# Optimization experiments

Measured on AMD Instinct MI355X. Metric: run time of the kernel, lower is better.

Reference implementation:

```python
import jax, jax.numpy as jnp
import numpy as np

N_NODES = 50000
N_EDGES = 400000
IN_DIM, HID_DIM, OUT_DIM = 512, 512, 128


def sage_conv(x, src, dst, W_l, b_l, W_r, n_nodes):
    # PyG SAGEConv (mean aggr): out = lin_l(mean_{j in N(i)} x_j) + lin_r(x_i)
    msgs = x[src]                                             # [E, d_in]
    agg = jax.ops.segment_sum(msgs, dst, num_segments=n_nodes)
    deg = jax.ops.segment_sum(jnp.ones((src.shape[0],), x.dtype), dst,
                              num_segments=n_nodes)
    mean = agg / jnp.maximum(deg, 1.0)[:, None]
    return mean @ W_l + b_l + x @ W_r


def setup_inputs() -> dict:
    key = jax.random.key(0)
    ks = jax.random.split(key, 9)
    x = jax.random.normal(ks[0], (N_NODES, IN_DIM), dtype=jnp.float32)
    edge_index = jax.random.randint(ks[1], (2, N_EDGES), 0, N_NODES, dtype=jnp.int32)

    def glorot(k, d_in, d_out):
        s = (6.0 / (d_in + d_out)) ** 0.5
        return jax.random.uniform(k, (d_in, d_out), jnp.float32, -s, s)

    return {
        "x": x,
        "edge_index": edge_index,
        "W1_l": glorot(ks[2], IN_DIM, HID_DIM),
        "b1": jnp.zeros((HID_DIM,), jnp.float32),
        "W1_r": glorot(ks[3], IN_DIM, HID_DIM),
        "W2_l": glorot(ks[4], HID_DIM, HID_DIM),
        "b2": jnp.zeros((HID_DIM,), jnp.float32),
        "W2_r": glorot(ks[5], HID_DIM, HID_DIM),
        "W3_l": glorot(ks[6], HID_DIM, OUT_DIM),
        "b3": jnp.zeros((OUT_DIM,), jnp.float32),
        "W3_r": glorot(ks[7], HID_DIM, OUT_DIM),
    }


def reference(x, edge_index, W1_l, b1, W1_r, W2_l, b2, W2_r, W3_l, b3, W3_r):
    src, dst = edge_index[0], edge_index[1]
    n = x.shape[0]
    h = sage_conv(x, src, dst, W1_l, b1, W1_r, n)
    h = jax.nn.relu(h)  # dropout is identity in eval mode
    h = sage_conv(h, src, dst, W2_l, b2, W2_r, n)
    h = jax.nn.relu(h)
    h = sage_conv(h, src, dst, W3_l, b3, W3_r, n)
    return jax.nn.log_softmax(h, axis=-1)
```

## Files before the change

### kernel.cpp

```cpp
#include <hip/hip_runtime.h>
#include <hip/hip_bf16.h>


#define N_NODES 50000
#define N_EDGES 400000

typedef unsigned short u16;
typedef unsigned int u32;
typedef __attribute__((ext_vector_type(8))) short short8;
typedef __attribute__((ext_vector_type(4))) float floatx4;

#define ASYNC16(g, l)                                                      \
    __builtin_amdgcn_global_load_lds(                                      \
        (const __attribute__((address_space(1))) void*)(g),                \
        (__attribute__((address_space(3))) void*)(l), 16, 0, 0)

__device__ __forceinline__ u16 f32_to_bf16(float f) {
    u32 u = __float_as_uint(f);
    u32 r = 0x7FFFu + ((u >> 16) & 1u);
    return (u16)((u + r) >> 16);
}
__device__ __forceinline__ float bf16_to_f32(u32 lo16) {
    return __uint_as_float(lo16 << 16);
}

__global__ __launch_bounds__(256) void zero4_kernel(float4* __restrict__ p, int n4) {
    int i = blockIdx.x * 256 + threadIdx.x;
    if (i < n4) p[i] = make_float4(0.f, 0.f, 0.f, 0.f);
}

__global__ __launch_bounds__(256) void hist_kernel(const int* __restrict__ dst,
                                                   int* __restrict__ deg, int E) {
    int e = blockIdx.x * 256 + threadIdx.x;
    if (e < E) atomicAdd(&deg[dst[e]], 1);
}

__global__ __launch_bounds__(256) void scan_reduce(const int* __restrict__ v,
                                                   int* __restrict__ bsums, int n) {
    __shared__ int sh[256];
    int i = blockIdx.x * 256 + threadIdx.x;
    sh[threadIdx.x] = (i < n) ? v[i] : 0;
    __syncthreads();
    for (int off = 128; off > 0; off >>= 1) {
        if (threadIdx.x < off) sh[threadIdx.x] += sh[threadIdx.x + off];
        __syncthreads();
    }
    if (threadIdx.x == 0) bsums[blockIdx.x] = sh[0];
}

__global__ __launch_bounds__(256) void scan_sums(int* __restrict__ bsums, int nb) {
    __shared__ int sh[256];
    int t = threadIdx.x;
    int val = (t < nb) ? bsums[t] : 0;
    sh[t] = val;
    __syncthreads();
    for (int off = 1; off < 256; off <<= 1) {
        int v = (t >= off) ? sh[t - off] : 0;
        __syncthreads();
        sh[t] += v;
        __syncthreads();
    }
    if (t < nb) bsums[t] = sh[t] - val;
}

__global__ __launch_bounds__(256) void scan_final(int* __restrict__ v,
                                                  const int* __restrict__ bsums, int n) {
    __shared__ int sh[256];
    int t = threadIdx.x;
    int i = blockIdx.x * 256 + t;
    int val = (i < n) ? v[i] : 0;
    sh[t] = val;
    __syncthreads();
    for (int off = 1; off < 256; off <<= 1) {
        int x = (t >= off) ? sh[t - off] : 0;
        __syncthreads();
        sh[t] += x;
        __syncthreads();
    }
    int excl = sh[t] - val + bsums[blockIdx.x];
    if (i < n) v[i] = excl;
    if (i == n - 1) v[n] = excl + val;
}

__global__ __launch_bounds__(256) void fill_kernel(const int* __restrict__ src,
                                                   const int* __restrict__ dst,
                                                   const int* __restrict__ row_start,
                                                   int* __restrict__ cursor,
                                                   int* __restrict__ csr_src, int E) {
    int e = blockIdx.x * 256 + threadIdx.x;
    if (e < E) {
        int d = dst[e];
        int pos = row_start[d] + atomicAdd(&cursor[d], 1);
        csr_src[pos] = src[e];
    }
}

__global__ __launch_bounds__(256) void convert_bf16(const float* __restrict__ in,
                                                    u16* __restrict__ out, int n8) {
    int i = blockIdx.x * 256 + threadIdx.x;
    if (i >= n8) return;
    const float4* p = (const float4*)in + (size_t)i * 2;
    float4 v0 = p[0], v1 = p[1];
    uint4 o;
    o.x = (u32)f32_to_bf16(v0.x) | ((u32)f32_to_bf16(v0.y) << 16);
    o.y = (u32)f32_to_bf16(v0.z) | ((u32)f32_to_bf16(v0.w) << 16);
    o.z = (u32)f32_to_bf16(v1.x) | ((u32)f32_to_bf16(v1.y) << 16);
    o.w = (u32)f32_to_bf16(v1.z) | ((u32)f32_to_bf16(v1.w) << 16);
    ((uint4*)out)[i] = o;
}

__global__ __launch_bounds__(256) void transpose_w(const float* __restrict__ W,
                                                   u16* __restrict__ WT,
                                                   int K, int N) {
    __shared__ float t[32][33];
    int n0 = blockIdx.x * 32, k0 = blockIdx.y * 32;
    int c = threadIdx.x & 31, r0 = threadIdx.x >> 5;
    for (int r = r0; r < 32; r += 8)
        t[r][c] = W[(size_t)(k0 + r) * N + n0 + c];
    __syncthreads();
    for (int r = r0; r < 32; r += 8)
        WT[(size_t)(n0 + r) * K + k0 + c] = f32_to_bf16(t[c][r]);
}

__global__ __launch_bounds__(256) void gemm_bf16(
    const u16* __restrict__ A, const u16* __restrict__ BT,
    u16* __restrict__ Cl, u16* __restrict__ Cr,
    int M, int split, int nStrips, int nCols) {
    __shared__ u16 As[2][4096];
    __shared__ u16 Bs[2][4096];

    const int grp = 8 * nCols;
    int b = blockIdx.x;
    int strip = (b / grp) * 8 + (b & 7);
    int colt = (b % grp) >> 3;
    if (strip >= nStrips) return;
    const int row0 = strip * 128, col0 = colt * 128;

    const int t = threadIdx.x;
    const int w = t >> 6, lane = t & 63;
    const int wm = (w >> 1) * 64, wn = (w & 1) * 64;
    const int l15 = lane & 15, kq = lane >> 4;
    const int swz = (l15 >> 1) & 3;

    floatx4 acc[4][4];
#pragma unroll
    for (int i = 0; i < 4; ++i)
#pragma unroll
        for (int j = 0; j < 4; ++j) acc[i][j] = floatx4{0.f, 0.f, 0.f, 0.f};

    const int sr = t >> 2;
    const int sc = t & 3;
    const int swzS = (sr >> 1) & 3;
    const size_t aA0 = (size_t)min(row0 + sr, M - 1) * 512 + (sc ^ swzS) * 8;
    const size_t aA1 = (size_t)min(row0 + 64 + sr, M - 1) * 512 + (sc ^ swzS) * 8;
    const size_t aB0 = (size_t)(col0 + sr) * 512 + (sc ^ swzS) * 8;
    const size_t aB1 = (size_t)(col0 + 64 + sr) * 512 + (sc ^ swzS) * 8;
    const int d0 = w * 512;
    const int d1 = 2048 + w * 512;

    auto stage = [&](int it, int buf) {
        const int eff = it * 32;
        ASYNC16(A + aA0 + eff, &As[buf][d0]);
        ASYNC16(A + aA1 + eff, &As[buf][d1]);
        ASYNC16(BT + aB0 + eff, &Bs[buf][d0]);
        ASYNC16(BT + aB1 + eff, &Bs[buf][d1]);
    };

    stage(0, 0);
    __syncthreads();
    for (int it = 0; it < 16; ++it) {
        const int buf = it & 1;
        if (it + 1 < 16) stage(it + 1, buf ^ 1);

        const int kc = (kq ^ swz) * 8;
        short8 a[4], bfr[4];
#pragma unroll
        for (int mt = 0; mt < 4; ++mt)
            a[mt] = *(const short8*)&As[buf][(wm + mt * 16 + l15) * 32 + kc];
#pragma unroll
        for (int nt = 0; nt < 4; ++nt)
            bfr[nt] = *(const short8*)&Bs[buf][(wn + nt * 16 + l15) * 32 + kc];
#pragma unroll
        for (int mt = 0; mt < 4; ++mt)
#pragma unroll
            for (int nt = 0; nt < 4; ++nt)
                acc[mt][nt] = __builtin_amdgcn_mfma_f32_16x16x32_bf16(
                    bfr[nt], a[mt], acc[mt][nt], 0, 0, 0);
        __syncthreads();
    }

    u16* __restrict__ Cbase = (col0 < split) ? Cl : Cr;
    const int cadj = (col0 < split) ? col0 : (col0 - split);
#pragma unroll
    for (int mt = 0; mt < 4; ++mt) {
        int row = row0 + wm + mt * 16 + l15;
        if (row >= M) continue;
#pragma unroll
        for (int nt = 0; nt < 4; ++nt) {
            int c0 = cadj + wn + nt * 16 + kq * 4;
            uint2 o;
            o.x = (u32)f32_to_bf16(acc[mt][nt][0]) |
                  ((u32)f32_to_bf16(acc[mt][nt][1]) << 16);
            o.y = (u32)f32_to_bf16(acc[mt][nt][2]) |
                  ((u32)f32_to_bf16(acc[mt][nt][3]) << 16);
            *(uint2*)(Cbase + (size_t)row * split + c0) = o;
        }
    }
}

__device__ __forceinline__ void acc8(float* a, uint4 v) {
    a[0] += bf16_to_f32(v.x & 0xffffu); a[1] += bf16_to_f32(v.x >> 16);
    a[2] += bf16_to_f32(v.y & 0xffffu); a[3] += bf16_to_f32(v.y >> 16);
    a[4] += bf16_to_f32(v.z & 0xffffu); a[5] += bf16_to_f32(v.z >> 16);
    a[6] += bf16_to_f32(v.w & 0xffffu); a[7] += bf16_to_f32(v.w >> 16);
}

__global__ __launch_bounds__(256) void gather_add_relu512(
    const u16* __restrict__ Yl, const u16* __restrict__ Yr,
    const float* __restrict__ bias,
    const int* __restrict__ row_start, const int* __restrict__ csr_src,
    u16* __restrict__ h, int M) {
    int node = (blockIdx.x * 256 + threadIdx.x) >> 6;
    int lane = threadIdx.x & 63;
    if (node >= M) return;
    int beg = row_start[node], end = row_start[node + 1];
    float a[8] = {0.f, 0.f, 0.f, 0.f, 0.f, 0.f, 0.f, 0.f};
    for (int c = beg; c < end; c += 64) {
        int nb = min(64, end - c);
        int eid = (lane < nb) ? csr_src[c + lane] : 0;
        int i = 0;
        for (; i + 4 <= nb; i += 4) {
            int s0 = __shfl(eid, i);
            int s1 = __shfl(eid, i + 1);
            int s2 = __shfl(eid, i + 2);
            int s3 = __shfl(eid, i + 3);
            uint4 v0 = ((const uint4*)(Yl + (size_t)s0 * 512))[lane];
            uint4 v1 = ((const uint4*)(Yl + (size_t)s1 * 512))[lane];
            uint4 v2 = ((const uint4*)(Yl + (size_t)s2 * 512))[lane];
            uint4 v3 = ((const uint4*)(Yl + (size_t)s3 * 512))[lane];
            acc8(a, v0); acc8(a, v1); acc8(a, v2); acc8(a, v3);
        }
        for (; i < nb; ++i) {
            int s = __shfl(eid, i);
            uint4 v = ((const uint4*)(Yl + (size_t)s * 512))[lane];
            acc8(a, v);
        }
    }
    float inv = 1.0f / fmaxf((float)(end - beg), 1.0f);
    uint4 yr = ((const uint4*)(Yr + (size_t)node * 512))[lane];
    float4 b0 = ((const float4*)bias)[lane * 2];
    float4 b1 = ((const float4*)bias)[lane * 2 + 1];
    float v0 = fmaxf(a[0] * inv + bf16_to_f32(yr.x & 0xffffu) + b0.x, 0.f);
    float v1 = fmaxf(a[1] * inv + bf16_to_f32(yr.x >> 16)     + b0.y, 0.f);
    float v2 = fmaxf(a[2] * inv + bf16_to_f32(yr.y & 0xffffu) + b0.z, 0.f);
    float v3 = fmaxf(a[3] * inv + bf16_to_f32(yr.y >> 16)     + b0.w, 0.f);
    float v4 = fmaxf(a[4] * inv + bf16_to_f32(yr.z & 0xffffu) + b1.x, 0.f);
    float v5 = fmaxf(a[5] * inv + bf16_to_f32(yr.z >> 16)     + b1.y, 0.f);
    float v6 = fmaxf(a[6] * inv + bf16_to_f32(yr.w & 0xffffu) + b1.z, 0.f);
    float v7 = fmaxf(a[7] * inv + bf16_to_f32(yr.w >> 16)     + b1.w, 0.f);
    uint4 o;
    o.x = (u32)f32_to_bf16(v0) | ((u32)f32_to_bf16(v1) << 16);
    o.y = (u32)f32_to_bf16(v2) | ((u32)f32_to_bf16(v3) << 16);
    o.z = (u32)f32_to_bf16(v4) | ((u32)f32_to_bf16(v5) << 16);
    o.w = (u32)f32_to_bf16(v6) | ((u32)f32_to_bf16(v7) << 16);
    ((uint4*)(h + (size_t)node * 512))[lane] = o;
}

__global__ __launch_bounds__(256) void gather_add_lsm128(
    const u16* __restrict__ Yl, const u16* __restrict__ Yr,
    const float* __restrict__ bias,
    const int* __restrict__ row_start, const int* __restrict__ csr_src,
    float* __restrict__ out, int M) {
    int node = blockIdx.x * 16 + (threadIdx.x >> 4);
    int lane = threadIdx.x & 63;
    int li = lane & 15;
    int gbase = lane & 48;
    if (node >= M) return;
    int beg = row_start[node], end = row_start[node + 1];
    float a[8] = {0.f, 0.f, 0.f, 0.f, 0.f, 0.f, 0.f, 0.f};
    for (int c = beg; c < end; c += 16) {
        int nb = min(16, end - c);
        int eid = (li < nb) ? csr_src[c + li] : 0;
        int i = 0;
        for (; i + 4 <= nb; i += 4) {
            int s0 = __shfl(eid, gbase + i);
            int s1 = __shfl(eid, gbase + i + 1);
            int s2 = __shfl(eid, gbase + i + 2);
            int s3 = __shfl(eid, gbase + i + 3);
            uint4 v0 = ((const uint4*)(Yl + (size_t)s0 * 128))[li];
            uint4 v1 = ((const uint4*)(Yl + (size_t)s1 * 128))[li];
            uint4 v2 = ((const uint4*)(Yl + (size_t)s2 * 128))[li];
            uint4 v3 = ((const uint4*)(Yl + (size_t)s3 * 128))[li];
            acc8(a, v0); acc8(a, v1); acc8(a, v2); acc8(a, v3);
        }
        for (; i < nb; ++i) {
            int s = __shfl(eid, gbase + i);
            uint4 v = ((const uint4*)(Yl + (size_t)s * 128))[li];
            acc8(a, v);
        }
    }
    float inv = 1.0f / fmaxf((float)(end - beg), 1.0f);
    uint4 yr = ((const uint4*)(Yr + (size_t)node * 128))[li];
    float4 b0 = ((const float4*)bias)[li * 2];
    float4 b1 = ((const float4*)bias)[li * 2 + 1];
    float v[8];
    v[0] = a[0] * inv + bf16_to_f32(yr.x & 0xffffu) + b0.x;
    v[1] = a[1] * inv + bf16_to_f32(yr.x >> 16)     + b0.y;
    v[2] = a[2] * inv + bf16_to_f32(yr.y & 0xffffu) + b0.z;
    v[3] = a[3] * inv + bf16_to_f32(yr.y >> 16)     + b0.w;
    v[4] = a[4] * inv + bf16_to_f32(yr.z & 0xffffu) + b1.x;
    v[5] = a[5] * inv + bf16_to_f32(yr.z >> 16)     + b1.y;
    v[6] = a[6] * inv + bf16_to_f32(yr.w & 0xffffu) + b1.z;
    v[7] = a[7] * inv + bf16_to_f32(yr.w >> 16)     + b1.w;
    float m = v[0];
#pragma unroll
    for (int j = 1; j < 8; ++j) m = fmaxf(m, v[j]);
#pragma unroll
    for (int off = 1; off < 16; off <<= 1) m = fmaxf(m, __shfl_xor(m, off));
    float s = 0.f;
#pragma unroll
    for (int j = 0; j < 8; ++j) s += expf(v[j] - m);
#pragma unroll
    for (int off = 1; off < 16; off <<= 1) s += __shfl_xor(s, off);
    float ls = m + logf(s);
    float* p = out + (size_t)node * 128 + li * 8;
    *(float4*)p       = make_float4(v[0] - ls, v[1] - ls, v[2] - ls, v[3] - ls);
    *(float4*)(p + 4) = make_float4(v[4] - ls, v[5] - ls, v[6] - ls, v[7] - ls);
}

extern "C" void kernel_launch(void* const* d_in, const int* in_sizes, int n_in,
                              void* d_out, int out_size, void* d_ws, size_t ws_size,
                              hipStream_t stream) {
    const float* x    = (const float*)d_in[0];
    const int*   ei   = (const int*)d_in[1];
    const float* W1_l = (const float*)d_in[2];
    const float* b1   = (const float*)d_in[3];
    const float* W1_r = (const float*)d_in[4];
    const float* W2_l = (const float*)d_in[5];
    const float* b2   = (const float*)d_in[6];
    const float* W2_r = (const float*)d_in[7];
    const float* W3_l = (const float*)d_in[8];
    const float* b3   = (const float*)d_in[9];
    const float* W3_r = (const float*)d_in[10];
    float* out = (float*)d_out;

    const int* src = ei;
    const int* dst = ei + N_EDGES;

    char* base = (char*)d_ws;
    int* row_start = (int*)(base);
    int* cursor    = (int*)(base + 200208);
    int* bsums     = (int*)(base + 400416);
    int* csr_src   = (int*)(base + 402464);
    u16* xb  = (u16*)(base + 2002464);
    u16* h1b = (u16*)(base + 53202464);
    u16* h2b = (u16*)(base + 104402464);
    u16* Yl  = (u16*)(base + 155602464);
    u16* Yr  = (u16*)(base + 206802464);
    u16* w1T = (u16*)(base + 258002464);
    u16* w2T = (u16*)(base + 259051040);
    u16* w3T = (u16*)(base + 260099616);

    const int E = N_EDGES, M = N_NODES;
    const int nblk = (M + 255) / 256;

    zero4_kernel<<<(25154 + 255) / 256, 256, 0, stream>>>((float4*)d_ws, 25154);
    hist_kernel<<<(E + 255) / 256, 256, 0, stream>>>(dst, row_start, E);
    scan_reduce<<<nblk, 256, 0, stream>>>(row_start, bsums, M);
    scan_sums<<<1, 256, 0, stream>>>(bsums, nblk);
    scan_final<<<nblk, 256, 0, stream>>>(row_start, bsums, M);
    fill_kernel<<<(E + 255) / 256, 256, 0, stream>>>(src, dst, row_start, cursor,
                                                     csr_src, E);

    convert_bf16<<<(3200000 + 255) / 256, 256, 0, stream>>>(x, xb, 3200000);
    transpose_w<<<dim3(16, 16), 256, 0, stream>>>(W1_l, w1T, 512, 512);
    transpose_w<<<dim3(16, 16), 256, 0, stream>>>(W1_r, w1T + 512 * 512, 512, 512);
    transpose_w<<<dim3(16, 16), 256, 0, stream>>>(W2_l, w2T, 512, 512);
    transpose_w<<<dim3(16, 16), 256, 0, stream>>>(W2_r, w2T + 512 * 512, 512, 512);
    transpose_w<<<dim3(4, 16), 256, 0, stream>>>(W3_l, w3T, 512, 128);
    transpose_w<<<dim3(4, 16), 256, 0, stream>>>(W3_r, w3T + 128 * 512, 512, 128);

    const int nStrips = (M + 127) / 128;
    const int grid8 = ((nStrips + 7) / 8) * 64;
    const int grid2 = ((nStrips + 7) / 8) * 16;
    const int gblocks = (M * 64 + 255) / 256;
    const int g16blocks = (M + 15) / 16;

    gemm_bf16<<<grid8, 256, 0, stream>>>(xb, w1T, Yl, Yr, M, 512, nStrips, 8);
    gather_add_relu512<<<gblocks, 256, 0, stream>>>(Yl, Yr, b1, row_start,
                                                    csr_src, h1b, M);
    gemm_bf16<<<grid8, 256, 0, stream>>>(h1b, w2T, Yl, Yr, M, 512, nStrips, 8);
    gather_add_relu512<<<gblocks, 256, 0, stream>>>(Yl, Yr, b2, row_start,
                                                    csr_src, h2b, M);
    gemm_bf16<<<grid2, 256, 0, stream>>>(h2b, w3T, Yl, Yr, M, 128, nStrips, 2);
    gather_add_lsm128<<<g16blocks, 256, 0, stream>>>(Yl, Yr, b3, row_start,
                                                     csr_src, out, M);
}
```

Measured before the change: 656.9 us.

## Replace 128x128 GEMM with 256x256 tile, 512-thread, K=64 pipelined kernel

Replaces the 128x128-tile, 256-thread bf16 MFMA GEMM with a 256x256-tile, 512-thread (8 wave) kernel that stages K=64 slices into 128KB of dynamic LDS. Async global-to-LDS loads for the next slices are interleaved across four sub-phases of the MFMA loop with explicit vmcnt waits and barriers, and s_setprio raises priority around the MFMA bursts. The larger tile is meant to raise arithmetic intensity and cut global/LDS traffic per FLOP. In exchange it uses more registers and LDS, which may limit occupancy, and the third layer's 256-column output now has blocks straddling the Yl/Yr split. Tail rows waste more work because of the bigger strips.

```diff
diff --git a/kernel.cpp b/kernel.cpp
--- a/kernel.cpp
+++ b/kernel.cpp
@@ -122,88 +122,121 @@
         WT[(size_t)(n0 + r) * K + k0 + c] = f32_to_bf16(t[c][r]);
 }
 
-__global__ __launch_bounds__(256) void gemm_bf16(
+__global__ __launch_bounds__(512, 2) void gemm256(
     const u16* __restrict__ A, const u16* __restrict__ BT,
     u16* __restrict__ Cl, u16* __restrict__ Cr,
     int M, int split, int nStrips, int nCols) {
-    __shared__ u16 As[2][4096];
-    __shared__ u16 Bs[2][4096];
+    extern __shared__ u16 lds[];
 
     const int grp = 8 * nCols;
     int b = blockIdx.x;
     int strip = (b / grp) * 8 + (b & 7);
     int colt = (b % grp) >> 3;
     if (strip >= nStrips) return;
-    const int row0 = strip * 128, col0 = colt * 128;
+    const int row0 = strip * 256, col0 = colt * 256;
 
     const int t = threadIdx.x;
     const int w = t >> 6, lane = t & 63;
-    const int wm = (w >> 1) * 64, wn = (w & 1) * 64;
+    const int arow = (w >> 2) * 128;
+    const int bcol = (w & 3) * 64;
     const int l15 = lane & 15, kq = lane >> 4;
-    const int swz = (l15 >> 1) & 3;
-
-    floatx4 acc[4][4];
-#pragma unroll
-    for (int i = 0; i < 4; ++i)
+    const int rchunk = (kq ^ ((l15 >> 1) & 3)) * 8;
+
+    floatx4 acc[8][4];
+#pragma unroll
+    for (int i = 0; i < 8; ++i)
 #pragma unroll
         for (int j = 0; j < 4; ++j) acc[i][j] = floatx4{0.f, 0.f, 0.f, 0.f};
 
-    const int sr = t >> 2;
-    const int sc = t & 3;
-    const int swzS = (sr >> 1) & 3;
-    const size_t aA0 = (size_t)min(row0 + sr, M - 1) * 512 + (sc ^ swzS) * 8;
-    const size_t aA1 = (size_t)min(row0 + 64 + sr, M - 1) * 512 + (sc ^ swzS) * 8;
-    const size_t aB0 = (size_t)(col0 + sr) * 512 + (sc ^ swzS) * 8;
-    const size_t aB1 = (size_t)(col0 + 64 + sr) * 512 + (sc ^ swzS) * 8;
-    const int d0 = w * 512;
-    const int d1 = 2048 + w * 512;
-
-    auto stage = [&](int it, int buf) {
-        const int eff = it * 32;
-        ASYNC16(A + aA0 + eff, &As[buf][d0]);
-        ASYNC16(A + aA1 + eff, &As[buf][d1]);
-        ASYNC16(BT + aB0 + eff, &Bs[buf][d0]);
-        ASYNC16(BT + aB1 + eff, &Bs[buf][d1]);
+    auto stA = [&](int kt2, int i) {
+        const int rb = (w & 3) * 16 + (i & 1) * 64 + (w >> 2) * 128;
+        const int plane = i >> 1;
+        const size_t src = (size_t)min(row0 + rb + (lane >> 2), M - 1) * 512
+                         + kt2 * 64 + plane * 32
+                         + (((lane & 3) ^ ((lane >> 3) & 3)) * 8);
+        const int dst = (kt2 & 1) * 32768 + plane * 8192 + rb * 32;
+        ASYNC16(A + src, &lds[dst]);
     };
-
-    stage(0, 0);
-    __syncthreads();
-    for (int it = 0; it < 16; ++it) {
-        const int buf = it & 1;
-        if (it + 1 < 16) stage(it + 1, buf ^ 1);
-
-        const int kc = (kq ^ swz) * 8;
-        short8 a[4], bfr[4];
-#pragma unroll
-        for (int mt = 0; mt < 4; ++mt)
-            a[mt] = *(const short8*)&As[buf][(wm + mt * 16 + l15) * 32 + kc];
+    auto stB = [&](int kt2, int i) {
+        const int rb = (w & 3) * 16 + (i & 1) * 64 + (w >> 2) * 128;
+        const int plane = i >> 1;
+        const size_t src = (size_t)(col0 + rb + (lane >> 2)) * 512
+                         + kt2 * 64 + plane * 32
+                         + (((lane & 3) ^ ((lane >> 3) & 3)) * 8);
+        const int dst = (kt2 & 1) * 32768 + 16384 + plane * 8192 + rb * 32;
+        ASYNC16(BT + src, &lds[dst]);
+    };
+
+    stA(0, 0); stA(0, 1); stA(0, 2); stA(0, 3);
+    stB(0, 0); stB(0, 1); stB(0, 2); stB(0, 3);
+    stA(1, 0); stA(1, 2);
+    asm volatile("s_waitcnt vmcnt(2)" ::: "memory");
+    __builtin_amdgcn_s_barrier();
+
+    for (int kt = 0; kt < 8; ++kt) {
+        const int sA = (kt & 1) * 32768;
+        const int sB = sA + 16384;
+
+        short8 bfr[4][2];
 #pragma unroll
         for (int nt = 0; nt < 4; ++nt)
-            bfr[nt] = *(const short8*)&Bs[buf][(wn + nt * 16 + l15) * 32 + kc];
-#pragma unroll
-        for (int mt = 0; mt < 4; ++mt)
-#pragma unroll
-            for (int nt = 0; nt < 4; ++nt)
-                acc[mt][nt] = __builtin_amdgcn_mfma_f32_16x16x32_bf16(
-                    bfr[nt], a[mt], acc[mt][nt], 0, 0, 0);
-        __syncthreads();
-    }
-
-    u16* __restrict__ Cbase = (col0 < split) ? Cl : Cr;
-    const int cadj = (col0 < split) ? col0 : (col0 - split);
-#pragma unroll
-    for (int mt = 0; mt < 4; ++mt) {
-        int row = row0 + wm + mt * 16 + l15;
+#pragma unroll
+            for (int j = 0; j < 2; ++j)
+                bfr[nt][j] = *(const short8*)
+                    &lds[sB + j * 8192 + (bcol + nt * 16 + l15) * 32 + rchunk];
+
+#pragma unroll
+        for (int q = 0; q < 4; ++q) {
+            if (q == 0)      { if (kt + 1 < 8) { stA(kt + 1, 1); stA(kt + 1, 3); } }
+            else if (q == 1) { if (kt + 1 < 8) { stB(kt + 1, 0); stB(kt + 1, 2); } }
+            else if (q == 2) { if (kt + 1 < 8) { stB(kt + 1, 1); stB(kt + 1, 3); } }
+            else             { if (kt + 2 < 8) { stA(kt + 2, 0); stA(kt + 2, 2); } }
+
+            short8 afr[2][2];
+#pragma unroll
+            for (int m2 = 0; m2 < 2; ++m2)
+#pragma unroll
+                for (int j = 0; j < 2; ++j)
+                    afr[m2][j] = *(const short8*)
+                        &lds[sA + j * 8192
+                             + (arow + (q * 2 + m2) * 16 + l15) * 32 + rchunk];
+
+            __builtin_amdgcn_s_setprio(1);
+#pragma unroll
+            for (int m2 = 0; m2 < 2; ++m2)
+#pragma unroll
+                for (int nt = 0; nt < 4; ++nt)
+#pragma unroll
+                    for (int j = 0; j < 2; ++j)
+                        acc[q * 2 + m2][nt] = __builtin_amdgcn_mfma_f32_16x16x32_bf16(
+                            bfr[nt][j], afr[m2][j], acc[q * 2 + m2][nt], 0, 0, 0);
+            __builtin_amdgcn_s_setprio(0);
+
+            if (q < 3) {
+                __builtin_amdgcn_s_barrier();
+            } else if (kt < 7) {
+                if (kt + 2 < 8) asm volatile("s_waitcnt vmcnt(2)" ::: "memory");
+                else            asm volatile("s_waitcnt vmcnt(0)" ::: "memory");
+                __builtin_amdgcn_s_barrier();
+            }
+        }
+    }
+
+#pragma unroll
+    for (int mt = 0; mt < 8; ++mt) {
+        int row = row0 + arow + mt * 16 + l15;
         if (row >= M) continue;
 #pragma unroll
         for (int nt = 0; nt < 4; ++nt) {
-            int c0 = cadj + wn + nt * 16 + kq * 4;
+            int c0 = col0 + bcol + nt * 16 + kq * 4;
+            u16* __restrict__ Cbase = (c0 < split) ? Cl : Cr;
+            int cadj = (c0 < split) ? c0 : (c0 - split);
             uint2 o;
             o.x = (u32)f32_to_bf16(acc[mt][nt][0]) |
                   ((u32)f32_to_bf16(acc[mt][nt][1]) << 16);
             o.y = (u32)f32_to_bf16(acc[mt][nt][2]) |
                   ((u32)f32_to_bf16(acc[mt][nt][3]) << 16);
-            *(uint2*)(Cbase + (size_t)row * split + c0) = o;
+            *(uint2*)(Cbase + (size_t)row * split + cadj) = o;
         }
     }
 }
@@ -364,6 +397,13 @@
     const int E = N_EDGES, M = N_NODES;
     const int nblk = (M + 255) / 256;
 
+    static int attrSet = 0;
+    if (!attrSet) {
+        hipFuncSetAttribute((const void*)gemm256,
+                            hipFuncAttributeMaxDynamicSharedMemorySize, 131072);
+        attrSet = 1;
+    }
+
     zero4_kernel<<<(25154 + 255) / 256, 256, 0, stream>>>((float4*)d_ws, 25154);
     hist_kernel<<<(E + 255) / 256, 256, 0, stream>>>(dst, row_start, E);
     scan_reduce<<<nblk, 256, 0, stream>>>(row_start, bsums, M);
@@ -380,19 +420,19 @@
     transpose_w<<<dim3(4, 16), 256, 0, stream>>>(W3_l, w3T, 512, 128);
     transpose_w<<<dim3(4, 16), 256, 0, stream>>>(W3_r, w3T + 128 * 512, 512, 128);
 
-    const int nStrips = (M + 127) / 128;
-    const int grid8 = ((nStrips + 7) / 8) * 64;
-    const int grid2 = ((nStrips + 7) / 8) * 16;
+    const int nStrips = (M + 255) / 256;
+    const int grid12 = ((nStrips + 7) / 8) * 8 * 4;
+    const int grid3  = ((nStrips + 7) / 8) * 8 * 1;
     const int gblocks = (M * 64 + 255) / 256;
     const int g16blocks = (M + 15) / 16;
 
-    gemm_bf16<<<grid8, 256, 0, stream>>>(xb, w1T, Yl, Yr, M, 512, nStrips, 8);
+    gemm256<<<grid12, 512, 131072, stream>>>(xb, w1T, Yl, Yr, M, 512, nStrips, 4);
     gather_add_relu512<<<gblocks, 256, 0, stream>>>(Yl, Yr, b1, row_start,
                                                     csr_src, h1b, M);
-    gemm_bf16<<<grid8, 256, 0, stream>>>(h1b, w2T, Yl, Yr, M, 512, nStrips, 8);
+    gemm256<<<grid12, 512, 131072, stream>>>(h1b, w2T, Yl, Yr, M, 512, nStrips, 4);
     gather_add_relu512<<<gblocks, 256, 0, stream>>>(Yl, Yr, b2, row_start,
                                                     csr_src, h2b, M);
-    gemm_bf16<<<grid2, 256, 0, stream>>>(h2b, w3T, Yl, Yr, M, 128, nStrips, 2);
+    gemm256<<<grid3, 512, 131072, stream>>>(h2b, w3T, Yl, Yr, M, 128, nStrips, 1);
     gather_add_lsm128<<<g16blocks, 256, 0, stream>>>(Yl, Yr, b3, row_start,
                                                      csr_src, out, M);
 }
```

Measured after the change: 624.0 us. 1.05x faster.
